# Kernel optimization log

Hardware: AMD Instinct MI355X
Metric: run time of the kernel (lower is better)

The kernel has to match this reference:

```python
import jax, jax.numpy as jnp
import numpy as np
import math

VOCAB = 32000
D = 2048
H = 16
KVH = 4
HD = D // H          # 128
FF = 5632
L = 2
S = 2048
B = 1
EPS = 1e-5
ROPE_BASE = 10000.0


def setup_inputs() -> dict:
    key = jax.random.key(0)
    ks = jax.random.split(key, 12)
    sc = 0.02
    # RoPE table: [S, HD//2, 2] (cos, sin), matching precompute_freqs_cis
    inv = 1.0 / (ROPE_BASE ** (jnp.arange(0, HD, 2, dtype=jnp.float32) / HD))
    pos = jnp.arange(S, dtype=jnp.float32)
    f = jnp.outer(pos, inv)
    freqs_cis = jnp.stack([jnp.cos(f), jnp.sin(f)], axis=-1)
    mask = jnp.tril(jnp.ones((S, S), dtype=bool))
    return {
        "input_ids": jax.random.randint(ks[0], (B, S), 0, VOCAB, dtype=jnp.int32),
        "mask": mask,
        "freqs_cis": freqs_cis,
        "w_embed": jax.random.normal(ks[1], (VOCAB, D), jnp.float32) * sc,
        "wqkv": jax.random.normal(ks[2], (L, D, D + 2 * KVH * HD), jnp.float32) * sc,
        "wo": jax.random.normal(ks[3], (L, D, D), jnp.float32) * sc,
        "w1": jax.random.normal(ks[4], (L, D, FF), jnp.float32) * sc,
        "w3": jax.random.normal(ks[5], (L, D, FF), jnp.float32) * sc,
        "w2": jax.random.normal(ks[6], (L, FF, D), jnp.float32) * sc,
        "attn_norm_w": jnp.ones((L, D), jnp.float32),
        "ff_norm_w": jnp.ones((L, D), jnp.float32),
        "final_norm_w": jnp.ones((D,), jnp.float32),
        "w_head": jax.random.normal(ks[7], (D, VOCAB), jnp.float32) * sc,
    }


def _rmsnorm(x, w):
    xf = x.astype(jnp.float32)
    n = xf * jax.lax.rsqrt(jnp.mean(xf * xf, axis=-1, keepdims=True) + EPS)
    return n.astype(x.dtype) * w


def _rope(x, fc):
    # x: [b, h, s, hd]; fc: [s, hd/2, 2]
    xr = x.reshape(*x.shape[:-1], HD // 2, 2)
    cos, sin = fc[..., 0], fc[..., 1]  # [s, hd/2] broadcast over b,h
    out = jnp.stack([xr[..., 0] * cos - xr[..., 1] * sin,
                     xr[..., 1] * cos + xr[..., 0] * sin], axis=-1)
    return out.reshape(x.shape).astype(x.dtype)


def _attention(x, mask, fc, wqkv, wo):
    b, s, _ = x.shape
    qkv = x @ wqkv  # [b, s, D + 2*kv_dim]
    kv_dim = KVH * HD
    q, k, v = jnp.split(qkv, [D, D + kv_dim], axis=-1)
    q = q.reshape(b, s, H, HD).transpose(0, 2, 1, 3)      # [b,H,s,hd]
    k = k.reshape(b, s, KVH, HD).transpose(0, 2, 1, 3)    # [b,KVH,s,hd]
    v = v.reshape(b, s, KVH, HD).transpose(0, 2, 1, 3)
    q = _rope(q, fc)
    k = _rope(k, fc)
    rep = H // KVH
    k = jnp.repeat(k, rep, axis=1)  # [b,H,s,hd]
    v = jnp.repeat(v, rep, axis=1)
    scores = jnp.einsum('bhqd,bhkd->bhqk', q, k) / math.sqrt(HD)
    scores = jnp.where(mask, scores, -1e30)
    attn = jax.nn.softmax(scores, axis=-1)
    out = jnp.einsum('bhqk,bhkd->bhqd', attn, v)
    out = out.transpose(0, 2, 1, 3).reshape(b, s, D)
    return out @ wo


def reference(input_ids, mask, freqs_cis, w_embed, wqkv, wo, w1, w3, w2,
              attn_norm_w, ff_norm_w, final_norm_w, w_head):
    x = w_embed[input_ids]  # [B,S,D]
    for l in range(L):
        h = x + _attention(_rmsnorm(x, attn_norm_w[l]), mask, freqs_cis,
                           wqkv[l], wo[l])
        hn = _rmsnorm(h, ff_norm_w[l])
        x = h + (jax.nn.silu(hn @ w1[l]) * (hn @ w3[l])) @ w2[l]
    x = _rmsnorm(x, final_norm_w)
    return x @ w_head  # [B,S,VOCAB]
```

## Files before the change

### kernel.cpp

```cpp
#include <hip/hip_runtime.h>

#define DD 2048
#define SEQ 2048
#define NH 16
#define NKV 4
#define HD 128
#define FFD 5632
#define NL 2

typedef __bf16 bf16x8 __attribute__((ext_vector_type(8)));
typedef float f32x4 __attribute__((ext_vector_type(4)));

#define AS1 __attribute__((address_space(1)))
#define AS3 __attribute__((address_space(3)))

__device__ __forceinline__ unsigned short f2bf(float f) {
    unsigned int u = __builtin_bit_cast(unsigned int, f);
    u += 0x7fffu + ((u >> 16) & 1u);
    return (unsigned short)(u >> 16);
}

__global__ __launch_bounds__(256)
void embed_gather(const int* __restrict__ ids, const float* __restrict__ wemb,
                  float* __restrict__ x)
{
    int s = blockIdx.x;
    int id = ids[s];
    const float4* src = (const float4*)(wemb + (size_t)id * DD);
    float4* dst = (float4*)(x + (size_t)s * DD);
    dst[threadIdx.x] = src[threadIdx.x];
    dst[threadIdx.x + 256] = src[threadIdx.x + 256];
}

__global__ __launch_bounds__(256)
void rmsnorm_bf16(const float* __restrict__ x, const float* __restrict__ w,
                  unsigned short* __restrict__ out)
{
    int row = blockIdx.x;
    int t = threadIdx.x;
    const float4* xr = (const float4*)(x + (size_t)row * DD);
    float4 v0 = xr[t], v1 = xr[t + 256];
    float ss = v0.x * v0.x + v0.y * v0.y + v0.z * v0.z + v0.w * v0.w
             + v1.x * v1.x + v1.y * v1.y + v1.z * v1.z + v1.w * v1.w;
#pragma unroll
    for (int off = 32; off; off >>= 1) ss += __shfl_down(ss, off);
    __shared__ float red[4];
    if ((t & 63) == 0) red[t >> 6] = ss;
    __syncthreads();
    float sc = rsqrtf((red[0] + red[1] + red[2] + red[3]) * (1.0f / DD) + 1e-5f);
    const float4* wr = (const float4*)w;
    float4 w0 = wr[t], w1v = wr[t + 256];
    ushort4 o0, o1;
    o0.x = f2bf(v0.x * sc * w0.x);  o0.y = f2bf(v0.y * sc * w0.y);
    o0.z = f2bf(v0.z * sc * w0.z);  o0.w = f2bf(v0.w * sc * w0.w);
    o1.x = f2bf(v1.x * sc * w1v.x); o1.y = f2bf(v1.y * sc * w1v.y);
    o1.z = f2bf(v1.z * sc * w1v.z); o1.w = f2bf(v1.w * sc * w1v.w);
    ushort4* op = (ushort4*)(out + (size_t)row * DD);
    op[t] = o0;
    op[t + 256] = o1;
}

__global__ __launch_bounds__(256)
void transpose_cast(const float* __restrict__ src, unsigned short* __restrict__ dst,
                    int ld_src, int ld_dst, size_t sb, size_t db, int nmap)
{
    __shared__ float tile[64][65];
    src += (size_t)blockIdx.z * sb;
    dst += (size_t)blockIdx.z * db;
    int c0 = blockIdx.x * 64, r0 = blockIdx.y * 64;
    int tx = threadIdx.x & 15, ty = threadIdx.x >> 4;
#pragma unroll
    for (int i = 0; i < 4; ++i) {
        int r = ty + i * 16;
        float4 v = *(const float4*)(src + (size_t)(r0 + r) * ld_src + c0 + tx * 4);
        tile[r][tx * 4 + 0] = v.x; tile[r][tx * 4 + 1] = v.y;
        tile[r][tx * 4 + 2] = v.z; tile[r][tx * 4 + 3] = v.w;
    }
    __syncthreads();
#pragma unroll
    for (int i = 0; i < 4; ++i) {
        int c = ty + i * 16;
        int cc = c0 + c;
        int dr = cc;
        if (nmap == 1) dr = ((cc >> 4) << 5) | (cc & 15);
        else if (nmap == 2) dr = (((cc >> 4) << 5) | (cc & 15)) + 16;
        ushort4 o;
        o.x = f2bf(tile[tx * 4 + 0][c]); o.y = f2bf(tile[tx * 4 + 1][c]);
        o.z = f2bf(tile[tx * 4 + 2][c]); o.w = f2bf(tile[tx * 4 + 3][c]);
        *(ushort4*)(dst + (size_t)dr * ld_dst + r0 + tx * 4) = o;
    }
}

__global__ void rope_qk(const float* __restrict__ qkv, const float* __restrict__ fc,
                        unsigned short* __restrict__ Qb, unsigned short* __restrict__ Kb)
{
    const float QSCL = 0.12751741530217758f;
    int s = blockIdx.x;
    int hh = blockIdx.y;
    int i = threadIdx.x;
    float2 cs = *(const float2*)(fc + ((size_t)s * 64 + i) * 2);
    const float* src;
    unsigned short* dst;
    float scl;
    if (hh < NH) {
        src = qkv + (size_t)s * 3072 + hh * HD;
        dst = Qb + ((size_t)hh * SEQ + s) * HD;
        scl = QSCL;
    } else {
        int kh = hh - NH;
        src = qkv + (size_t)s * 3072 + DD + kh * HD;
        dst = Kb + ((size_t)kh * SEQ + s) * HD;
        scl = 1.0f;
    }
    float2 xv = *(const float2*)(src + 2 * i);
    ushort2 o;
    o.x = f2bf((xv.x * cs.x - xv.y * cs.y) * scl);
    o.y = f2bf((xv.y * cs.x + xv.x * cs.y) * scl);
    *(ushort2*)(dst + 2 * i) = o;
}

__global__ __launch_bounds__(256)
void gemm_bf16(const unsigned short* __restrict__ A, const unsigned short* __restrict__ B,
               float* __restrict__ C, const float* __restrict__ Res,
               int N, int K, int mT)
{
    __shared__ __attribute__((aligned(16))) unsigned char smem[65536];
    const int tid = threadIdx.x;
    const int lane = tid & 63;
    const int w = tid >> 6;
    const int nwg = gridDim.x;
    const int qq = nwg >> 3;
    const int logical = ((int)blockIdx.x & 7) * qq + ((int)blockIdx.x >> 3);
    const int m0 = (logical % mT) * 128;
    const int n0 = (logical / mT) * 128;
    const int wm = (w >> 1) * 64, wn = (w & 1) * 64;
    const int lrow = lane & 15, lgrp = lane >> 4;
    const int NT = K >> 6;

    f32x4 acc[4][4];
#pragma unroll
    for (int i = 0; i < 4; ++i)
#pragma unroll
        for (int j = 0; j < 4; ++j) acc[i][j] = 0.f;

    auto stage = [&](int bsel, int kt) {
#pragma unroll
        for (int it = 0; it < 4; ++it) {
            int o = it * 4096 + tid * 16;
            int row = o >> 7;
            int col = (o & 127) ^ ((row & 7) << 4);
            const char* ga = (const char*)A + ((size_t)(m0 + row) * K + kt) * 2 + col;
            const char* gb = (const char*)B + ((size_t)(n0 + row) * K + kt) * 2 + col;
            __builtin_amdgcn_global_load_lds(
                (AS1 const void*)ga,
                (AS3 void*)(smem + bsel * 32768 + it * 4096 + w * 1024),
                16, 0, 0);
            __builtin_amdgcn_global_load_lds(
                (AS1 const void*)gb,
                (AS3 void*)(smem + bsel * 32768 + 16384 + it * 4096 + w * 1024),
                16, 0, 0);
        }
    };

    stage(0, 0);
    int cur = 0;
    for (int t = 0; t < NT; ++t) {
        if (t + 1 < NT) {
            stage(cur ^ 1, (t + 1) << 6);
            asm volatile("s_waitcnt vmcnt(8)" ::: "memory");
        } else {
            asm volatile("s_waitcnt vmcnt(0)" ::: "memory");
        }
        __builtin_amdgcn_s_barrier();
        __builtin_amdgcn_sched_barrier(0);
        const unsigned char* buf = smem + cur * 32768;
#pragma unroll
        for (int kk = 0; kk < 2; ++kk) {
            bf16x8 af[4], bfr[4];
            int cb = kk * 64 + lgrp * 16;
#pragma unroll
            for (int i = 0; i < 4; ++i) {
                int ra = wm + i * 16 + lrow;
                af[i] = *(const bf16x8*)(buf + ra * 128 + (cb ^ ((ra & 7) << 4)));
                int rb = wn + i * 16 + lrow;
                bfr[i] = *(const bf16x8*)(buf + 16384 + rb * 128 + (cb ^ ((rb & 7) << 4)));
            }
#pragma unroll
            for (int i = 0; i < 4; ++i)
#pragma unroll
                for (int j = 0; j < 4; ++j)
                    acc[i][j] = __builtin_amdgcn_mfma_f32_16x16x32_bf16(af[i], bfr[j], acc[i][j], 0, 0, 0);
        }
        __builtin_amdgcn_s_barrier();
        cur ^= 1;
    }

    const bool hasRes = (Res != nullptr);
#pragma unroll
    for (int i = 0; i < 4; ++i)
#pragma unroll
        for (int j = 0; j < 4; ++j) {
            int r = m0 + wm + i * 16 + lgrp * 4;
            int c = n0 + wn + j * 16 + lrow;
#pragma unroll
            for (int jj = 0; jj < 4; ++jj) {
                size_t idx = (size_t)(r + jj) * N + c;
                float v = acc[i][j][jj];
                if (hasRes) v += Res[idx];
                C[idx] = v;
            }
        }
}

template<int FUSE>
__global__ __launch_bounds__(512, 1)
void gemm_bf16_256(const unsigned short* __restrict__ A, const unsigned short* __restrict__ B,
                   void* __restrict__ Cout, int N, int K, int mT)
{
    __shared__ __attribute__((aligned(16))) unsigned char smem[131072];
    const int tid = threadIdx.x;
    const int lane = tid & 63;
    const int w = tid >> 6;
    const int nwg = gridDim.x;
    const int qq = nwg >> 3;
    const int logical = ((int)blockIdx.x & 7) * qq + ((int)blockIdx.x >> 3);
    const int m0 = (logical % mT) * 256;
    const int n0 = (logical / mT) * 256;
    const int wm2 = (w >> 2) * 128;
    const int lrow = lane & 15, lgrp = (lane >> 4) & 3;
    const int NT = K >> 5;

    f32x4 acc[8][4];
#pragma unroll
    for (int i = 0; i < 8; ++i)
#pragma unroll
        for (int j = 0; j < 4; ++j) acc[i][j] = 0.f;

    const int X = (((lrow & 1) << 6) | (lgrp << 4)) ^ ((lrow >> 1) << 4);
    const int aoff = ((wm2 >> 1) + (lrow >> 1)) * 128 + X;
    const int boff = 16384 + (((w & 3) * 32) + (lrow >> 1)) * 128 + X;

    auto stage_part = [&](int ktile, int part) {
        const unsigned short* base = part ? B : A;
        const int r0 = part ? n0 : m0;
        const int ktb = ktile << 6;
#pragma unroll
        for (int j = 0; j < 2; ++j) {
            int o = j * 8192 + tid * 16;
            int p = o >> 7;
            int sl = (o & 127) ^ ((p & 7) << 4);
            int r = 2 * p + (sl >> 6);
            int cb = sl & 63;
            const char* g = (const char*)base + (size_t)(r0 + r) * K * 2 + ktb + cb;
            __builtin_amdgcn_global_load_lds(
                (AS1 const void*)g,
                (AS3 void*)(smem + (ktile & 3) * 32768 + part * 16384 + o),
                16, 0, 0);
        }
    };

    bf16x8 bE[4], aE[4], bO[4], aO[4], a47[4];

    auto read_ba = [&](int t, bf16x8* bs, bf16x8* as) {
        const unsigned char* buf = smem + (t & 3) * 32768;
#pragma unroll
        for (int nj = 0; nj < 4; ++nj) bs[nj] = *(const bf16x8*)(buf + boff + nj * 1024);
#pragma unroll
        for (int mi = 0; mi < 4; ++mi) as[mi] = *(const bf16x8*)(buf + aoff + mi * 1024);
    };

    auto tile = [&](int t, bf16x8* bc, bf16x8* ac, bf16x8* bn, bf16x8* an) {
        const unsigned char* buf = smem + (t & 3) * 32768;
        if (t + 3 < NT) stage_part(t + 3, 0);
#pragma unroll
        for (int mi = 0; mi < 4; ++mi) a47[mi] = *(const bf16x8*)(buf + aoff + (mi + 4) * 1024);
        asm volatile("s_waitcnt lgkmcnt(4)" ::: "memory");
        __builtin_amdgcn_sched_barrier(0);
        __builtin_amdgcn_s_setprio(1);
#pragma unroll
        for (int mi = 0; mi < 4; ++mi)
#pragma unroll
            for (int nj = 0; nj < 4; ++nj)
                acc[mi][nj] = __builtin_amdgcn_mfma_f32_16x16x32_bf16(ac[mi], bc[nj], acc[mi][nj], 0, 0, 0);
        __builtin_amdgcn_s_setprio(0);
        if (t + 3 < NT) stage_part(t + 3, 1);
        if (t + 1 < NT) {
            if (t + 3 < NT)      { asm volatile("s_waitcnt vmcnt(8)" ::: "memory"); }
            else if (t + 2 < NT) { asm volatile("s_waitcnt vmcnt(4)" ::: "memory"); }
            else                 { asm volatile("s_waitcnt vmcnt(0)" ::: "memory"); }
            __builtin_amdgcn_s_barrier();
            __builtin_amdgcn_sched_barrier(0);
            read_ba(t + 1, bn, an);
            asm volatile("s_waitcnt lgkmcnt(8)" ::: "memory");
        } else {
            asm volatile("s_waitcnt lgkmcnt(0)" ::: "memory");
        }
        __builtin_amdgcn_sched_barrier(0);
        __builtin_amdgcn_s_setprio(1);
#pragma unroll
        for (int mi = 0; mi < 4; ++mi)
#pragma unroll
            for (int nj = 0; nj < 4; ++nj)
                acc[mi + 4][nj] = __builtin_amdgcn_mfma_f32_16x16x32_bf16(a47[mi], bc[nj], acc[mi + 4][nj], 0, 0, 0);
        __builtin_amdgcn_s_setprio(0);
    };

#pragma unroll
    for (int p0 = 0; p0 < 3; ++p0) { stage_part(p0, 0); stage_part(p0, 1); }
    asm volatile("s_waitcnt vmcnt(8)" ::: "memory");
    __builtin_amdgcn_s_barrier();
    __builtin_amdgcn_sched_barrier(0);
    read_ba(0, bE, aE);

    for (int tt = 0; tt < NT; tt += 2) {
        tile(tt, bE, aE, bO, aO);
        tile(tt + 1, bO, aO, bE, aE);
    }

    if constexpr (FUSE == 0) {
        float* C = (float*)Cout;
#pragma unroll
        for (int mi = 0; mi < 8; ++mi)
#pragma unroll
            for (int nj = 0; nj < 4; ++nj) {
                int r = m0 + wm2 + mi * 16 + lgrp * 4;
                int c = n0 + (w & 3) * 64 + nj * 16 + lrow;
#pragma unroll
                for (int jj = 0; jj < 4; ++jj)
                    C[(size_t)(r + jj) * N + c] = acc[mi][nj][jj];
            }
    } else {
        unsigned short* G = (unsigned short*)Cout;
        const int nbase = n0 + (w & 3) * 64;
#pragma unroll
        for (int mi = 0; mi < 8; ++mi)
#pragma unroll
            for (int p = 0; p < 2; ++p) {
                int r = m0 + wm2 + mi * 16 + lgrp * 4;
                int cc = (nbase >> 1) + p * 16 + lrow;
#pragma unroll
                for (int jj = 0; jj < 4; ++jj) {
                    float h1 = acc[mi][2 * p][jj];
                    float h3 = acc[mi][2 * p + 1][jj];
                    float g = h1 / (1.f + __expf(-h1)) * h3;
                    G[(size_t)(r + jj) * FFD + cc] = f2bf(g);
                }
            }
    }
}

__global__ __launch_bounds__(256)
void attn_fwd(const unsigned short* __restrict__ Qb, const unsigned short* __restrict__ Kb,
              const unsigned short* __restrict__ VTb, unsigned short* __restrict__ O)
{
    __shared__ __attribute__((aligned(16))) unsigned char smem[73728];
    const int bid = (int)blockIdx.x;
    const int j0 = bid & 255;
    const int h = j0 & 15;
    const int qbase = j0 >> 4;
    const int qb = (bid >> 8) ? (31 - qbase) : qbase;
    const int kvh = h >> 2;
    const int tid = threadIdx.x, lane = tid & 63, w = tid >> 6;
    const int lrow = lane & 15, lgrp = lane >> 4;
    const int q0 = qb * 64 + w * 16;
    const float NEG = -1.0e30f;

    bf16x8 qf[4];
    const unsigned short* qrow = Qb + ((size_t)h * SEQ + q0 + lrow) * HD;
#pragma unroll
    for (int c = 0; c < 4; ++c)
        qf[c] = *(const bf16x8*)(qrow + c * 32 + lgrp * 8);

    float m[4], l[4];
    f32x4 oacc[8];
#pragma unroll
    for (int j = 0; j < 8; ++j) oacc[j] = 0.f;
#pragma unroll
    for (int j = 0; j < 4; ++j) { m[j] = NEG; l[j] = 0.f; }

    const char* kbase = (const char*)(Kb + (size_t)kvh * SEQ * HD);
    const char* vbase = (const char*)(VTb + (size_t)kvh * HD * SEQ);
    unsigned char* Pl = smem + 65536 + w * 2048;

    auto stage_kv = [&](int bsel, int t) {
#pragma unroll
        for (int it = 0; it < 4; ++it) {
            int o = it * 4096 + tid * 16;
            int row = o >> 8, col = o & 255;
            int scol = col ^ ((row & 7) << 4);
            const char* g = kbase + (size_t)(t * 64 + row) * 256 + scol;
            __builtin_amdgcn_global_load_lds(
                (AS1 const void*)g,
                (AS3 void*)(smem + bsel * 32768 + it * 4096 + w * 1024),
                16, 0, 0);
        }
#pragma unroll
        for (int it = 0; it < 4; ++it) {
            int o = it * 4096 + tid * 16;
            int row = o >> 7, col = o & 127;
            int scol = col ^ ((row & 7) << 4);
            const char* g = vbase + (size_t)row * (SEQ * 2) + (size_t)t * 128 + scol;
            __builtin_amdgcn_global_load_lds(
                (AS1 const void*)g,
                (AS3 void*)(smem + bsel * 32768 + 16384 + it * 4096 + w * 1024),
                16, 0, 0);
        }
    };

    stage_kv(0, 0);
    int cur = 0;
    for (int t = 0; t <= qb; ++t) {
        if (t < qb) {
            stage_kv(cur ^ 1, t + 1);
            asm volatile("s_waitcnt vmcnt(8)" ::: "memory");
        } else {
            asm volatile("s_waitcnt vmcnt(0)" ::: "memory");
        }
        __builtin_amdgcn_s_barrier();
        __builtin_amdgcn_sched_barrier(0);
        const unsigned char* kb = smem + cur * 32768;
        const unsigned char* vtb = kb + 16384;

        f32x4 sf[4];
#pragma unroll
        for (int kf = 0; kf < 4; ++kf) sf[kf] = 0.f;
#pragma unroll
        for (int kf = 0; kf < 4; ++kf) {
            int rb = kf * 16 + lrow;
            int rbase = rb * 256;
            int sw = (rb & 7) << 4;
#pragma unroll
            for (int c = 0; c < 4; ++c) {
                bf16x8 kfr = *(const bf16x8*)(kb + rbase + ((c * 64 + lgrp * 16) ^ sw));
                sf[kf] = __builtin_amdgcn_mfma_f32_16x16x32_bf16(qf[c], kfr, sf[kf], 0, 0, 0);
            }
        }
        const bool diag = (t == qb);
        float mx[4] = {NEG, NEG, NEG, NEG};
#pragma unroll
        for (int kf = 0; kf < 4; ++kf)
#pragma unroll
            for (int j = 0; j < 4; ++j) {
                float v = sf[kf][j];
                if (diag && (t * 64 + kf * 16 + lrow) > (q0 + lgrp * 4 + j)) v = NEG;
                sf[kf][j] = v;
                mx[j] = fmaxf(mx[j], v);
            }
#pragma unroll
        for (int off = 1; off < 16; off <<= 1)
#pragma unroll
            for (int j = 0; j < 4; ++j) mx[j] = fmaxf(mx[j], __shfl_xor(mx[j], off));
        bool need = (mx[0] > m[0] + 8.f) || (mx[1] > m[1] + 8.f) ||
                    (mx[2] > m[2] + 8.f) || (mx[3] > m[3] + 8.f);
        if (__any(need)) {
#pragma unroll
            for (int j = 0; j < 4; ++j) {
                float mn = fmaxf(m[j], mx[j]);
                float al = exp2f(m[j] - mn);
                m[j] = mn;
                l[j] *= al;
#pragma unroll
                for (int hf = 0; hf < 8; ++hf) oacc[hf][j] *= al;
            }
        }
        float rs[4] = {0.f, 0.f, 0.f, 0.f};
#pragma unroll
        for (int kf = 0; kf < 4; ++kf)
#pragma unroll
            for (int j = 0; j < 4; ++j) {
                float p = exp2f(sf[kf][j] - m[j]);
                rs[j] += p;
                int qq = lgrp * 4 + j;
                int addr = qq * 128 + (((kf * 16 + lrow) * 2) ^ ((qq & 7) << 4));
                *(unsigned short*)(Pl + addr) = f2bf(p);
            }
#pragma unroll
        for (int off = 1; off < 16; off <<= 1)
#pragma unroll
            for (int j = 0; j < 4; ++j) rs[j] += __shfl_xor(rs[j], off);
#pragma unroll
        for (int j = 0; j < 4; ++j) l[j] += rs[j];
#pragma unroll
        for (int c = 0; c < 2; ++c) {
            int cb = c * 64 + lgrp * 16;
            bf16x8 pf = *(const bf16x8*)(Pl + lrow * 128 + (cb ^ ((lrow & 7) << 4)));
#pragma unroll
            for (int hf = 0; hf < 8; ++hf) {
                int rv = hf * 16 + lrow;
                bf16x8 vf = *(const bf16x8*)(vtb + rv * 128 + (cb ^ ((rv & 7) << 4)));
                oacc[hf] = __builtin_amdgcn_mfma_f32_16x16x32_bf16(pf, vf, oacc[hf], 0, 0, 0);
            }
        }
        __builtin_amdgcn_s_barrier();
        cur ^= 1;
    }
#pragma unroll
    for (int hf = 0; hf < 8; ++hf)
#pragma unroll
        for (int j = 0; j < 4; ++j) {
            float v = oacc[hf][j] / l[j];
            int qg = q0 + lgrp * 4 + j;
            O[(size_t)qg * DD + h * HD + hf * 16 + lrow] = f2bf(v);
        }
}

extern "C" void kernel_launch(void* const* d_in, const int* in_sizes, int n_in,
                              void* d_out, int out_size, void* d_ws, size_t ws_size,
                              hipStream_t stream)
{
    (void)in_sizes; (void)n_in; (void)out_size; (void)ws_size;
    const int* ids = (const int*)d_in[0];
    const float* fc   = (const float*)d_in[2];
    const float* wemb = (const float*)d_in[3];
    const float* wqkv = (const float*)d_in[4];
    const float* wo   = (const float*)d_in[5];
    const float* w1   = (const float*)d_in[6];
    const float* w3   = (const float*)d_in[7];
    const float* w2   = (const float*)d_in[8];
    const float* anw  = (const float*)d_in[9];
    const float* fnw  = (const float*)d_in[10];
    const float* finw = (const float*)d_in[11];
    const float* wh   = (const float*)d_in[12];
    float* out = (float*)d_out;
    char* ws = (char*)d_ws;

    unsigned short* WQKVT = (unsigned short*)(ws);
    unsigned short* WOT   = (unsigned short*)(ws + 25165824);
    unsigned short* W13T  = (unsigned short*)(ws + 41943040);
    unsigned short* W2T   = (unsigned short*)(ws + 134217728);
    unsigned short* WHT   = (unsigned short*)(ws + 180355072);
    float*          X     = (float*)(ws + 311427072);
    unsigned short* XN    = (unsigned short*)(ws + 328204288);
    float*          QKV   = (float*)(ws + 336592896);
    unsigned short* Qb    = (unsigned short*)(ws + 361758720);
    unsigned short* Kb    = (unsigned short*)(ws + 370147328);
    unsigned short* VT    = (unsigned short*)(ws + 372244480);
    unsigned short* AO    = (unsigned short*)(ws + 374341632);
    unsigned short* G     = (unsigned short*)(ws + 475004928);

    transpose_cast<<<dim3(48, 32, 2), 256, 0, stream>>>(wqkv, WQKVT, 3072, 2048,
        (size_t)2048 * 3072, (size_t)3072 * 2048, 0);
    transpose_cast<<<dim3(32, 32, 2), 256, 0, stream>>>(wo, WOT, 2048, 2048,
        (size_t)2048 * 2048, (size_t)2048 * 2048, 0);
    transpose_cast<<<dim3(88, 32, 2), 256, 0, stream>>>(w1, W13T, 5632, 2048,
        (size_t)2048 * 5632, (size_t)11264 * 2048, 1);
    transpose_cast<<<dim3(88, 32, 2), 256, 0, stream>>>(w3, W13T, 5632, 2048,
        (size_t)2048 * 5632, (size_t)11264 * 2048, 2);
    transpose_cast<<<dim3(32, 88, 2), 256, 0, stream>>>(w2, W2T, 2048, 5632,
        (size_t)5632 * 2048, (size_t)2048 * 5632, 0);
    transpose_cast<<<dim3(500, 32, 1), 256, 0, stream>>>(wh, WHT, 32000, 2048, 0, 0, 0);

    embed_gather<<<dim3(SEQ), 256, 0, stream>>>(ids, wemb, X);

    for (int lyr = 0; lyr < NL; ++lyr) {
        const unsigned short* wqkvT_l = WQKVT + (size_t)lyr * 3072 * 2048;
        const unsigned short* woT_l   = WOT   + (size_t)lyr * 2048 * 2048;
        const unsigned short* w13T_l  = W13T  + (size_t)lyr * 11264 * 2048;
        const unsigned short* w2T_l   = W2T   + (size_t)lyr * 2048 * 5632;

        rmsnorm_bf16<<<dim3(SEQ), 256, 0, stream>>>(X, anw + lyr * DD, XN);
        gemm_bf16<<<dim3(24 * 16), 256, 0, stream>>>(XN, wqkvT_l, QKV, nullptr, 3072, 2048, 16);
        rope_qk<<<dim3(SEQ, NH + NKV), 64, 0, stream>>>(QKV, fc, Qb, Kb);
        transpose_cast<<<dim3(2, 32, 4), 256, 0, stream>>>(QKV + 2560, VT, 3072, 2048,
            128, (size_t)128 * 2048, 0);
        attn_fwd<<<dim3(512), 256, 0, stream>>>(Qb, Kb, VT, AO);
        gemm_bf16<<<dim3(16 * 16), 256, 0, stream>>>(AO, woT_l, X, X, 2048, 2048, 16);
        rmsnorm_bf16<<<dim3(SEQ), 256, 0, stream>>>(X, fnw + lyr * DD, XN);
        gemm_bf16_256<1><<<dim3(8 * 44), 512, 0, stream>>>(XN, w13T_l, G, 11264, 2048, 8);
        gemm_bf16<<<dim3(16 * 16), 256, 0, stream>>>(G, w2T_l, X, X, 2048, 5632, 16);
    }
    rmsnorm_bf16<<<dim3(SEQ), 256, 0, stream>>>(X, finw, XN);
    gemm_bf16_256<0><<<dim3(8 * 125), 512, 0, stream>>>(XN, WHT, out, 32000, 2048, 8);
}
```

Measured before the change: 1.182 ms.

## Load V fragments directly into registers, stage only K through LDS

The attention kernel no longer stages V^T tiles through shared memory. Each wave loads its V fragments straight from global memory into registers, and only K stays double-buffered in LDS, which cuts LDS from 72KB to 40KB. The aim is to raise occupancy and remove the LDS write/read round trip for V. It also adds s_setprio around the MFMA sections and retunes the vmcnt waits. The trade-off is that each wave now issues redundant global loads of V and holds more registers (16 bf16x8 fragments).

```diff
diff --git a/kernel.cpp b/kernel.cpp
--- a/kernel.cpp
+++ b/kernel.cpp
@@ -353,7 +353,7 @@
 void attn_fwd(const unsigned short* __restrict__ Qb, const unsigned short* __restrict__ Kb,
               const unsigned short* __restrict__ VTb, unsigned short* __restrict__ O)
 {
-    __shared__ __attribute__((aligned(16))) unsigned char smem[73728];
+    __shared__ __attribute__((aligned(16))) unsigned char smem[40960];
     const int bid = (int)blockIdx.x;
     const int j0 = bid & 255;
     const int h = j0 & 15;
@@ -380,9 +380,9 @@
 
     const char* kbase = (const char*)(Kb + (size_t)kvh * SEQ * HD);
     const char* vbase = (const char*)(VTb + (size_t)kvh * HD * SEQ);
-    unsigned char* Pl = smem + 65536 + w * 2048;
-
-    auto stage_kv = [&](int bsel, int t) {
+    unsigned char* Pl = smem + 32768 + w * 2048;
+
+    auto stage_k = [&](int bsel, int t) {
 #pragma unroll
         for (int it = 0; it < 4; ++it) {
             int o = it * 4096 + tid * 16;
@@ -391,39 +391,32 @@
             const char* g = kbase + (size_t)(t * 64 + row) * 256 + scol;
             __builtin_amdgcn_global_load_lds(
                 (AS1 const void*)g,
-                (AS3 void*)(smem + bsel * 32768 + it * 4096 + w * 1024),
+                (AS3 void*)(smem + bsel * 16384 + o),
                 16, 0, 0);
         }
-#pragma unroll
-        for (int it = 0; it < 4; ++it) {
-            int o = it * 4096 + tid * 16;
-            int row = o >> 7, col = o & 127;
-            int scol = col ^ ((row & 7) << 4);
-            const char* g = vbase + (size_t)row * (SEQ * 2) + (size_t)t * 128 + scol;
-            __builtin_amdgcn_global_load_lds(
-                (AS1 const void*)g,
-                (AS3 void*)(smem + bsel * 32768 + 16384 + it * 4096 + w * 1024),
-                16, 0, 0);
-        }
     };
 
-    stage_kv(0, 0);
+    stage_k(0, 0);
     int cur = 0;
     for (int t = 0; t <= qb; ++t) {
-        if (t < qb) {
-            stage_kv(cur ^ 1, t + 1);
-            asm volatile("s_waitcnt vmcnt(8)" ::: "memory");
-        } else {
-            asm volatile("s_waitcnt vmcnt(0)" ::: "memory");
-        }
+        if (t < qb) stage_k(cur ^ 1, t + 1);
+        bf16x8 vf[2][8];
+#pragma unroll
+        for (int c = 0; c < 2; ++c)
+#pragma unroll
+            for (int hf = 0; hf < 8; ++hf)
+                vf[c][hf] = *(const bf16x8*)(vbase +
+                    (size_t)(hf * 16 + lrow) * (SEQ * 2) + (size_t)t * 128 + c * 64 + lgrp * 16);
+        if (t < qb) { asm volatile("s_waitcnt vmcnt(20)" ::: "memory"); }
+        else        { asm volatile("s_waitcnt vmcnt(16)" ::: "memory"); }
         __builtin_amdgcn_s_barrier();
         __builtin_amdgcn_sched_barrier(0);
-        const unsigned char* kb = smem + cur * 32768;
-        const unsigned char* vtb = kb + 16384;
+        const unsigned char* kb = smem + cur * 16384;
 
         f32x4 sf[4];
 #pragma unroll
         for (int kf = 0; kf < 4; ++kf) sf[kf] = 0.f;
+        __builtin_amdgcn_s_setprio(1);
 #pragma unroll
         for (int kf = 0; kf < 4; ++kf) {
             int rb = kf * 16 + lrow;
@@ -435,6 +428,7 @@
                 sf[kf] = __builtin_amdgcn_mfma_f32_16x16x32_bf16(qf[c], kfr, sf[kf], 0, 0, 0);
             }
         }
+        __builtin_amdgcn_s_setprio(0);
         const bool diag = (t == qb);
         float mx[4] = {NEG, NEG, NEG, NEG};
 #pragma unroll
@@ -480,17 +474,19 @@
             for (int j = 0; j < 4; ++j) rs[j] += __shfl_xor(rs[j], off);
 #pragma unroll
         for (int j = 0; j < 4; ++j) l[j] += rs[j];
+        if (t < qb) { asm volatile("s_waitcnt vmcnt(4)" ::: "memory"); }
+        else        { asm volatile("s_waitcnt vmcnt(0)" ::: "memory"); }
+        __builtin_amdgcn_sched_barrier(0);
+        __builtin_amdgcn_s_setprio(1);
 #pragma unroll
         for (int c = 0; c < 2; ++c) {
             int cb = c * 64 + lgrp * 16;
             bf16x8 pf = *(const bf16x8*)(Pl + lrow * 128 + (cb ^ ((lrow & 7) << 4)));
 #pragma unroll
-            for (int hf = 0; hf < 8; ++hf) {
-                int rv = hf * 16 + lrow;
-                bf16x8 vf = *(const bf16x8*)(vtb + rv * 128 + (cb ^ ((rv & 7) << 4)));
-                oacc[hf] = __builtin_amdgcn_mfma_f32_16x16x32_bf16(pf, vf, oacc[hf], 0, 0, 0);
-            }
-        }
+            for (int hf = 0; hf < 8; ++hf)
+                oacc[hf] = __builtin_amdgcn_mfma_f32_16x16x32_bf16(pf, vf[c][hf], oacc[hf], 0, 0, 0);
+        }
+        __builtin_amdgcn_s_setprio(0);
         __builtin_amdgcn_s_barrier();
         cur ^= 1;
     }
```

Result: slower. 1.285 ms (+8.7%).

## Fuse head weight fp32-to-bf16 conversion into LM-head GEMM B loading

Applied to the files above, without the earlier changes.

Drops the separate transpose/cast pass over the 32000x2048 fp32 head weight. A new 256x256 GEMM kernel instead reads fp32 B rows directly from global memory into registers, converts them to bf16 and writes them into swizzled LDS. A is still staged with direct global-to-LDS loads in a 4-buffer pipeline. This removes one full weight read and write and a kernel launch. In exchange the GEMM reads twice as many B bytes and does conversion work in its main loop.

```diff
diff --git a/kernel.cpp b/kernel.cpp
--- a/kernel.cpp
+++ b/kernel.cpp
@@ -349,6 +349,162 @@
     }
 }
 
+__global__ __launch_bounds__(512, 1)
+void gemm_b32_256(const unsigned short* __restrict__ A, const float* __restrict__ Bf,
+                  float* __restrict__ C, int N, int K, int mT)
+{
+    __shared__ __attribute__((aligned(16))) unsigned char smem[131072];
+    const int tid = threadIdx.x;
+    const int lane = tid & 63;
+    const int w = tid >> 6;
+    const int nwg = gridDim.x;
+    const int qq = nwg >> 3;
+    const int logical = ((int)blockIdx.x & 7) * qq + ((int)blockIdx.x >> 3);
+    const int m0 = (logical % mT) * 256;
+    const int n0 = (logical / mT) * 256;
+    const int wm2 = (w >> 2) * 128;
+    const int lrow = lane & 15, lgrp = (lane >> 4) & 3;
+    const int NT = K >> 5;
+
+    f32x4 acc[8][4];
+#pragma unroll
+    for (int i = 0; i < 8; ++i)
+#pragma unroll
+        for (int j = 0; j < 4; ++j) acc[i][j] = 0.f;
+
+    const int X = (((lrow & 1) << 6) | (lgrp << 4)) ^ ((lrow >> 1) << 4);
+    const int aoff = ((wm2 >> 1) + (lrow >> 1)) * 128 + X;
+    const int boff = 16384 + (((w & 3) * 32) + (lrow >> 1)) * 128 + X;
+
+    auto stage_A = [&](int ktile) {
+        const int ktb = ktile << 6;
+#pragma unroll
+        for (int j = 0; j < 2; ++j) {
+            int o = j * 8192 + tid * 16;
+            int p = o >> 7;
+            int sl = (o & 127) ^ ((p & 7) << 4);
+            int r = 2 * p + (sl >> 6);
+            int cb = sl & 63;
+            const char* g = (const char*)A + (size_t)(m0 + r) * K * 2 + ktb + cb;
+            __builtin_amdgcn_global_load_lds(
+                (AS1 const void*)g,
+                (AS3 void*)(smem + (ktile & 3) * 32768 + o),
+                16, 0, 0);
+        }
+    };
+
+    const int nb4 = (tid & 63) * 4;
+    const int k0 = (tid >> 6) * 4;
+
+    auto loadB = [&](float4* f, int x) {
+        const float* src = Bf + (size_t)(x * 32 + k0) * N + n0 + nb4;
+#pragma unroll
+        for (int j = 0; j < 4; ++j) f[j] = *(const float4*)(src + (size_t)j * N);
+    };
+
+    auto writeB = [&](float4* f, int x) {
+        unsigned char* dst = smem + (x & 3) * 32768 + 16384;
+#pragma unroll
+        for (int i = 0; i < 4; ++i) {
+            int n = nb4 + i;
+            int p = n >> 1, hi = n & 1;
+            unsigned short h0 = f2bf(((const float*)&f[0])[i]);
+            unsigned short h1 = f2bf(((const float*)&f[1])[i]);
+            unsigned short h2 = f2bf(((const float*)&f[2])[i]);
+            unsigned short h3 = f2bf(((const float*)&f[3])[i]);
+            uint2 v;
+            v.x = (unsigned)h0 | ((unsigned)h1 << 16);
+            v.y = (unsigned)h2 | ((unsigned)h3 << 16);
+            int sl = (hi << 6) | (k0 * 2);
+            *(uint2*)(dst + p * 128 + (sl ^ ((p & 7) << 4))) = v;
+        }
+    };
+
+    bf16x8 bE[4], aE[4], bO[4], aO[4], a47[4];
+    float4 fB0[4], fB1[4];
+
+    auto read_ba = [&](int t, bf16x8* bs, bf16x8* as) {
+        const unsigned char* buf = smem + (t & 3) * 32768;
+#pragma unroll
+        for (int nj = 0; nj < 4; ++nj) bs[nj] = *(const bf16x8*)(buf + boff + nj * 1024);
+#pragma unroll
+        for (int mi = 0; mi < 4; ++mi) as[mi] = *(const bf16x8*)(buf + aoff + mi * 1024);
+    };
+
+    auto tileF = [&](int t, bf16x8* bc, bf16x8* ac, bf16x8* bn, bf16x8* an,
+                     float4* fw, float4* fl) {
+        const unsigned char* buf = smem + (t & 3) * 32768;
+        const bool haveW = (t + 1 < NT);
+        if (haveW) {
+            if (t + 2 < NT) { asm volatile("s_waitcnt vmcnt(2)" ::: "memory"); }
+            else            { asm volatile("s_waitcnt vmcnt(0)" ::: "memory"); }
+            __builtin_amdgcn_sched_barrier(0);
+            writeB(fw, t + 1);
+        }
+        if (t + 2 < NT) loadB(fl, t + 2);
+        if (t + 3 < NT) stage_A(t + 3);
+#pragma unroll
+        for (int mi = 0; mi < 4; ++mi) a47[mi] = *(const bf16x8*)(buf + aoff + (mi + 4) * 1024);
+        if (haveW) { asm volatile("s_waitcnt lgkmcnt(8)" ::: "memory"); }
+        else       { asm volatile("s_waitcnt lgkmcnt(4)" ::: "memory"); }
+        __builtin_amdgcn_sched_barrier(0);
+        __builtin_amdgcn_s_setprio(1);
+#pragma unroll
+        for (int mi = 0; mi < 4; ++mi)
+#pragma unroll
+            for (int nj = 0; nj < 4; ++nj)
+                acc[mi][nj] = __builtin_amdgcn_mfma_f32_16x16x32_bf16(ac[mi], bc[nj], acc[mi][nj], 0, 0, 0);
+        __builtin_amdgcn_s_setprio(0);
+        if (haveW) {
+            asm volatile("s_waitcnt lgkmcnt(4)" ::: "memory");
+            __builtin_amdgcn_sched_barrier(0);
+            __builtin_amdgcn_s_barrier();
+            __builtin_amdgcn_sched_barrier(0);
+            read_ba(t + 1, bn, an);
+            asm volatile("s_waitcnt lgkmcnt(8)" ::: "memory");
+        } else {
+            asm volatile("s_waitcnt lgkmcnt(0)" ::: "memory");
+        }
+        __builtin_amdgcn_sched_barrier(0);
+        __builtin_amdgcn_s_setprio(1);
+#pragma unroll
+        for (int mi = 0; mi < 4; ++mi)
+#pragma unroll
+            for (int nj = 0; nj < 4; ++nj)
+                acc[mi + 4][nj] = __builtin_amdgcn_mfma_f32_16x16x32_bf16(a47[mi], bc[nj], acc[mi + 4][nj], 0, 0, 0);
+        __builtin_amdgcn_s_setprio(0);
+    };
+
+    loadB(fB0, 0);
+    loadB(fB1, 1);
+    stage_A(0); stage_A(1); stage_A(2);
+    asm volatile("s_waitcnt vmcnt(10)" ::: "memory");
+    __builtin_amdgcn_sched_barrier(0);
+    writeB(fB0, 0);
+    asm volatile("s_waitcnt vmcnt(4)" ::: "memory");
+    asm volatile("s_waitcnt lgkmcnt(0)" ::: "memory");
+    __builtin_amdgcn_sched_barrier(0);
+    __builtin_amdgcn_s_barrier();
+    __builtin_amdgcn_sched_barrier(0);
+    read_ba(0, bE, aE);
+
+    for (int tt = 0; tt < NT; tt += 2) {
+        tileF(tt,     bE, aE, bO, aO, fB1, fB0);
+        tileF(tt + 1, bO, aO, bE, aE, fB0, fB1);
+    }
+
+#pragma unroll
+    for (int mi = 0; mi < 8; ++mi)
+#pragma unroll
+        for (int nj = 0; nj < 4; ++nj) {
+            int r = m0 + wm2 + mi * 16 + lgrp * 4;
+            int c = n0 + (w & 3) * 64 + nj * 16 + lrow;
+#pragma unroll
+            for (int jj = 0; jj < 4; ++jj)
+                C[(size_t)(r + jj) * N + c] = acc[mi][nj][jj];
+        }
+}
+
 __global__ __launch_bounds__(256)
 void attn_fwd(const unsigned short* __restrict__ Qb, const unsigned short* __restrict__ Kb,
               const unsigned short* __restrict__ VTb, unsigned short* __restrict__ O)
@@ -528,7 +684,6 @@
     unsigned short* WOT   = (unsigned short*)(ws + 25165824);
     unsigned short* W13T  = (unsigned short*)(ws + 41943040);
     unsigned short* W2T   = (unsigned short*)(ws + 134217728);
-    unsigned short* WHT   = (unsigned short*)(ws + 180355072);
     float*          X     = (float*)(ws + 311427072);
     unsigned short* XN    = (unsigned short*)(ws + 328204288);
     float*          QKV   = (float*)(ws + 336592896);
@@ -548,7 +703,6 @@
         (size_t)2048 * 5632, (size_t)11264 * 2048, 2);
     transpose_cast<<<dim3(32, 88, 2), 256, 0, stream>>>(w2, W2T, 2048, 5632,
         (size_t)5632 * 2048, (size_t)2048 * 5632, 0);
-    transpose_cast<<<dim3(500, 32, 1), 256, 0, stream>>>(wh, WHT, 32000, 2048, 0, 0, 0);
 
     embed_gather<<<dim3(SEQ), 256, 0, stream>>>(ids, wemb, X);
 
@@ -570,5 +724,5 @@
         gemm_bf16<<<dim3(16 * 16), 256, 0, stream>>>(G, w2T_l, X, X, 2048, 5632, 16);
     }
     rmsnorm_bf16<<<dim3(SEQ), 256, 0, stream>>>(X, finw, XN);
-    gemm_bf16_256<0><<<dim3(8 * 125), 512, 0, stream>>>(XN, WHT, out, 32000, 2048, 8);
-}
+    gemm_b32_256<<<dim3(8 * 125), 512, 0, stream>>>(XN, wh, out, 32000, 2048, 8);
+}
```

Result: slower. 1.548 ms (+30.9%).
